# Kernel optimization log

Hardware: AMD Instinct MI355X
Metric: run time of the kernel (lower is better)

The kernel has to match this reference:

```python
import jax, jax.numpy as jnp
import numpy as np

HEADS = 4
DIM_HEAD = 32
SCALE = DIM_HEAD ** (-0.5)


def setup_inputs() -> dict:
    key = jax.random.key(0)
    k0, k1, k2 = jax.random.split(key, 3)
    B, C, H, W = 4, 256, 64, 64
    inner = HEADS * DIM_HEAD  # 128
    x = jax.random.normal(k0, (B, C, H, W), dtype=jnp.float32)
    # 1x1 conv weights reduce to matrices (out_ch, in_ch)
    w_qkv = jax.random.normal(k1, (3 * inner, C), dtype=jnp.float32) * 0.02
    w_out = jax.random.normal(k2, (C, inner), dtype=jnp.float32) * 0.02
    b_out = jnp.zeros((C,), dtype=jnp.float32)
    return {"x": x, "w_qkv": w_qkv, "w_out": w_out, "b_out": b_out}


def reference(x, w_qkv, w_out, b_out):
    b, c, h, w = x.shape
    n = h * w  # flattened spatial length
    inner = HEADS * DIM_HEAD
    # 1x1 conv == channel matmul: [b, 3*inner, h, w]
    qkv = jnp.einsum('oc,bchw->bohw', w_qkv, x)
    qkv = qkv.reshape(b, 3, HEADS, DIM_HEAD, n)  # split 3 * (heads dim_head)
    q, k, v = qkv[:, 0], qkv[:, 1], qkv[:, 2]    # each [b, heads, d, n]
    sim = jnp.einsum('bhdi,bhdj->bhij', q * SCALE, k)  # [b, h, n, n]
    attn = jax.nn.softmax(sim, axis=-1)  # stable (max-subtract) softmax
    out = jnp.einsum('bhij,bhdj->bhid', attn, v)       # [b, heads, n, d]
    # 'b h (x y) d -> b (h d) x y'
    out = out.transpose(0, 1, 3, 2).reshape(b, inner, h, w)
    y = jnp.einsum('oc,bchw->bohw', w_out, out) + b_out[None, :, None, None]
    return y
```

## Files before the change

### kernel.cpp

```cpp
#include <hip/hip_runtime.h>

#define N_TOK 4096
#define BATCH 4

typedef __attribute__((ext_vector_type(8))) short short8;
typedef __attribute__((ext_vector_type(4))) float floatx4;

__device__ __forceinline__ unsigned pack_rnd(float a, float b) {
    unsigned ra = __float_as_uint(a) + 0x8000u;
    unsigned rb = __float_as_uint(b) + 0x8000u;
    return __builtin_amdgcn_perm(rb, ra, 0x07060302u);
}

__device__ __forceinline__ void split_pack(float a, float b,
                                           unsigned &ph, unsigned &pl) {
    unsigned ra = __float_as_uint(a) + 0x8000u;
    unsigned rb = __float_as_uint(b) + 0x8000u;
    ph = __builtin_amdgcn_perm(rb, ra, 0x07060302u);
    float la = a - __uint_as_float(ra & 0xffff0000u);
    float lb = b - __uint_as_float(rb & 0xffff0000u);
    pl = __builtin_amdgcn_perm(__float_as_uint(lb) + 0x8000u,
                               __float_as_uint(la) + 0x8000u, 0x07060302u);
}

__device__ __forceinline__ short8 mk_short8(unsigned p0, unsigned p1,
                                            unsigned p2, unsigned p3) {
    union { unsigned u[4]; short8 s; } c;
    c.u[0] = p0; c.u[1] = p1; c.u[2] = p2; c.u[3] = p3;
    return c.s;
}

__device__ __forceinline__ void cvt_frag(const float* src,
                                         short8 &hi, short8 &lo) {
    float4 w0 = *(const float4*)src;
    float4 w1 = *(const float4*)(src + 4);
    unsigned ph[4], pl[4];
    split_pack(w0.x, w0.y, ph[0], pl[0]);
    split_pack(w0.z, w0.w, ph[1], pl[1]);
    split_pack(w1.x, w1.y, ph[2], pl[2]);
    split_pack(w1.z, w1.w, ph[3], pl[3]);
    hi = mk_short8(ph[0], ph[1], ph[2], ph[3]);
    lo = mk_short8(pl[0], pl[1], pl[2], pl[3]);
}

__device__ __forceinline__ float fast_exp2(float x) {
#if __has_builtin(__builtin_amdgcn_exp2f)
    return __builtin_amdgcn_exp2f(x);
#else
    return exp2f(x);
#endif
}

__global__ __launch_bounds__(256) void gemm1_fused(
    const float* __restrict__ wq, const float* __restrict__ x,
    unsigned short* __restrict__ Qp, unsigned short* __restrict__ Kp,
    unsigned short* __restrict__ Vp)
{
    const int N = N_TOK;
    const int b = blockIdx.z;
    const int row0 = blockIdx.y * 64;
    const int col0 = blockIdx.x * 64;
    const int t = threadIdx.x;
    const int wave = t >> 6, lane = t & 63;
    const int l16 = lane & 15, quad = lane >> 4;
    const int msub0 = (wave & 1) * 32, nsub0 = (wave >> 1) * 32;

    __shared__ __align__(16) char smem[29184];
    float (*Xf)[68] = (float(*)[68])smem;
    unsigned short* XsH = (unsigned short*)(smem + 8704);
    unsigned short* XsL = (unsigned short*)(smem + 13824);
    unsigned short* WsH = (unsigned short*)(smem + 18944);
    unsigned short* WsL = (unsigned short*)(smem + 24064);

    floatx4 acc[2][2] = {};

    const int xr = t >> 3, xnb = (t & 7) * 8;
    const int tnr = t >> 2, tkb = (t & 3) * 8;
    const int wm = t >> 2, wk = (t & 3) * 8;

    for (int kc = 0; kc < 8; ++kc) {
        __syncthreads();
        {
            const float* wsrc = wq + (size_t)(row0 + wm) * 256 + kc * 32 + wk;
            float4 w0 = *(const float4*)wsrc;
            float4 w1 = *(const float4*)(wsrc + 4);
            unsigned ph[4], pl[4];
            split_pack(w0.x, w0.y, ph[0], pl[0]);
            split_pack(w0.z, w0.w, ph[1], pl[1]);
            split_pack(w1.x, w1.y, ph[2], pl[2]);
            split_pack(w1.z, w1.w, ph[3], pl[3]);
            *(uint4*)(WsH + wm * 40 + wk) = *(uint4*)ph;
            *(uint4*)(WsL + wm * 40 + wk) = *(uint4*)pl;
        }
        {
            const float* src = x + ((size_t)b * 256 + kc * 32 + xr) * N + col0 + xnb;
            *(float4*)&Xf[xr][xnb]     = *(const float4*)src;
            *(float4*)&Xf[xr][xnb + 4] = *(const float4*)(src + 4);
        }
        __syncthreads();
        {
            unsigned ph[4], pl[4];
#pragma unroll
            for (int q = 0; q < 4; ++q)
                split_pack(Xf[tkb + 2 * q][tnr], Xf[tkb + 2 * q + 1][tnr],
                           ph[q], pl[q]);
            *(uint4*)(XsH + tnr * 40 + tkb) = *(uint4*)ph;
            *(uint4*)(XsL + tnr * 40 + tkb) = *(uint4*)pl;
        }
        __syncthreads();
        short8 ah0 = *(const short8*)(WsH + (msub0 + l16) * 40 + quad * 8);
        short8 ah1 = *(const short8*)(WsH + (msub0 + 16 + l16) * 40 + quad * 8);
        short8 al0 = *(const short8*)(WsL + (msub0 + l16) * 40 + quad * 8);
        short8 al1 = *(const short8*)(WsL + (msub0 + 16 + l16) * 40 + quad * 8);
        short8 bh0 = *(const short8*)(XsH + (nsub0 + l16) * 40 + quad * 8);
        short8 bh1 = *(const short8*)(XsH + (nsub0 + 16 + l16) * 40 + quad * 8);
        short8 bl0 = *(const short8*)(XsL + (nsub0 + l16) * 40 + quad * 8);
        short8 bl1 = *(const short8*)(XsL + (nsub0 + 16 + l16) * 40 + quad * 8);
        acc[0][0] = __builtin_amdgcn_mfma_f32_16x16x32_bf16(ah0, bh0, acc[0][0], 0, 0, 0);
        acc[0][1] = __builtin_amdgcn_mfma_f32_16x16x32_bf16(ah0, bh1, acc[0][1], 0, 0, 0);
        acc[1][0] = __builtin_amdgcn_mfma_f32_16x16x32_bf16(ah1, bh0, acc[1][0], 0, 0, 0);
        acc[1][1] = __builtin_amdgcn_mfma_f32_16x16x32_bf16(ah1, bh1, acc[1][1], 0, 0, 0);
        acc[0][0] = __builtin_amdgcn_mfma_f32_16x16x32_bf16(ah0, bl0, acc[0][0], 0, 0, 0);
        acc[0][1] = __builtin_amdgcn_mfma_f32_16x16x32_bf16(ah0, bl1, acc[0][1], 0, 0, 0);
        acc[1][0] = __builtin_amdgcn_mfma_f32_16x16x32_bf16(ah1, bl0, acc[1][0], 0, 0, 0);
        acc[1][1] = __builtin_amdgcn_mfma_f32_16x16x32_bf16(ah1, bl1, acc[1][1], 0, 0, 0);
        acc[0][0] = __builtin_amdgcn_mfma_f32_16x16x32_bf16(al0, bh0, acc[0][0], 0, 0, 0);
        acc[0][1] = __builtin_amdgcn_mfma_f32_16x16x32_bf16(al0, bh1, acc[0][1], 0, 0, 0);
        acc[1][0] = __builtin_amdgcn_mfma_f32_16x16x32_bf16(al1, bh0, acc[1][0], 0, 0, 0);
        acc[1][1] = __builtin_amdgcn_mfma_f32_16x16x32_bf16(al1, bh1, acc[1][1], 0, 0, 0);
    }

    __syncthreads();
    const int region = row0 >> 7;
    if (region == 2) {
        float (*LdsF)[68] = (float(*)[68])smem;
#pragma unroll
        for (int i = 0; i < 2; ++i)
#pragma unroll
            for (int j = 0; j < 2; ++j) {
                const int m = msub0 + i * 16 + quad * 4;
                const int n = nsub0 + j * 16 + l16;
#pragma unroll
                for (int r = 0; r < 4; ++r) LdsF[m + r][n] = acc[i][j][r];
            }
        __syncthreads();
        const int m = t >> 2, nb2 = (t & 3) * 16;
        const int vrow = b * 128 + (row0 - 256) + m;
        unsigned pk[8];
#pragma unroll
        for (int q = 0; q < 8; ++q)
            pk[q] = pack_rnd(LdsF[m][nb2 + 2 * q], LdsF[m][nb2 + 2 * q + 1]);
        unsigned short* dst = Vp + (size_t)vrow * N + col0 + nb2;
        *(uint4*)&dst[0] = *(uint4*)&pk[0];
        *(uint4*)&dst[8] = *(uint4*)&pk[4];
    } else {
        unsigned short (*LdsT)[68] = (unsigned short(*)[68])smem;
        const float sc = region ? 1.0f
                                : (0.17677669529663687f * 1.4426950408889634f);
#pragma unroll
        for (int i = 0; i < 2; ++i)
#pragma unroll
            for (int j = 0; j < 2; ++j) {
                const int m = msub0 + i * 16 + quad * 4;
                const int n = nsub0 + j * 16 + l16;
                uint2 pr;
                pr.x = pack_rnd(acc[i][j][0] * sc, acc[i][j][1] * sc);
                pr.y = pack_rnd(acc[i][j][2] * sc, acc[i][j][3] * sc);
                *(uint2*)&LdsT[n][m] = pr;
            }
        __syncthreads();
        const int n = t & 63, hb = (t >> 6) & 1, dh = t >> 7;
        const int h = ((row0 & 127) >> 5) + hb;
        const int m0 = hb * 32 + dh * 16;
        unsigned tmp[8];
        *(uint2*)&tmp[0] = *(const uint2*)&LdsT[n][m0];
        *(uint2*)&tmp[2] = *(const uint2*)&LdsT[n][m0 + 4];
        *(uint2*)&tmp[4] = *(const uint2*)&LdsT[n][m0 + 8];
        *(uint2*)&tmp[6] = *(const uint2*)&LdsT[n][m0 + 12];
        unsigned short* dst = (region ? Kp : Qp) +
            ((size_t)(b * 4 + h) * N + col0 + n) * 32 + dh * 16;
        *(uint4*)&dst[0] = *(uint4*)&tmp[0];
        *(uint4*)&dst[8] = *(uint4*)&tmp[4];
    }
}

__global__ __launch_bounds__(512) void attn_fused(
    const unsigned short* __restrict__ Qp,
    const unsigned short* __restrict__ Kp,
    const unsigned short* __restrict__ Vp,
    unsigned short* __restrict__ Oth, unsigned short* __restrict__ Otl)
{
    const int N = N_TOK;
    const int bh = blockIdx.y;
    const int b = bh >> 2, h = bh & 3;
    const int i0 = blockIdx.x * 128;
    const int t = threadIdx.x;
    const int wave = t >> 6, lane = t & 63;
    const int l16 = lane & 15, quad = lane >> 4;
    const int team = wave >> 2, w4 = wave & 3;

    __shared__ __align__(16) char smem[38912];
    unsigned short* S = (unsigned short*)smem;

    short8 ones;
#pragma unroll
    for (int e = 0; e < 8; ++e) ones[e] = (short)0x3F80;

    short8 qh[2];
#pragma unroll
    for (int g = 0; g < 2; ++g)
        qh[g] = *(const short8*)(Qp +
            ((size_t)bh * N + i0 + w4 * 32 + g * 16 + l16) * 32 + quad * 8);

    floatx4 o[2][2] = {};
    floatx4 lacc[2] = {};

    const int st_k = t & 255;
    const int skey = st_k >> 2, sdp = (st_k & 3) * 8;
    const int sslot = (skey & 32) | ((skey & 4) << 2) | ((skey & 24) >> 1)
                    | (skey & 3);
    const int svd = st_k >> 3, svp = (st_k & 7) * 8;
    const unsigned short* kp0 = Kp + ((size_t)bh * N + skey) * 32 + sdp;
    const unsigned short* kp1 = kp0 + (size_t)2048 * 32;
    const unsigned short* vp0 = Vp + ((size_t)bh * 32 + svd) * N + svp;
    const unsigned short* vp1 = vp0 + 2048;

    short8 r0, r1;
    if (t < 256) { r0 = *(const short8*)kp0; r1 = *(const short8*)kp1; }
    else         { r0 = *(const short8*)vp0; r1 = *(const short8*)vp1; }
    if (t < 256) {
        *(short8*)(S + sslot * 40 + sdp) = r0;
        *(short8*)(S + 2560 + sslot * 40 + sdp) = r1;
    } else {
        *(short8*)(S + 10240 + svd * 72 + svp) = r0;
        *(short8*)(S + 10240 + 2304 + svd * 72 + svp) = r1;
    }
    kp0 += 64 * 32; kp1 += 64 * 32; vp0 += 64; vp1 += 64;
    if (t < 256) { r0 = *(const short8*)kp0; r1 = *(const short8*)kp1; }
    else         { r0 = *(const short8*)vp0; r1 = *(const short8*)vp1; }
    __syncthreads();

    for (int it = 0; it < 32; ++it) {
        const int cur = it & 1;
        if (it + 1 < 32) {
            const int nb = 1 - cur;
            if (t < 256) {
                *(short8*)(S + nb * 5120 + sslot * 40 + sdp) = r0;
                *(short8*)(S + nb * 5120 + 2560 + sslot * 40 + sdp) = r1;
            } else {
                *(short8*)(S + 10240 + nb * 4608 + svd * 72 + svp) = r0;
                *(short8*)(S + 10240 + nb * 4608 + 2304 + svd * 72 + svp) = r1;
            }
        }
        if (it + 2 < 32) {
            kp0 += 64 * 32; kp1 += 64 * 32; vp0 += 64; vp1 += 64;
            if (t < 256) { r0 = *(const short8*)kp0; r1 = *(const short8*)kp1; }
            else         { r0 = *(const short8*)vp0; r1 = *(const short8*)vp1; }
        }

        const unsigned short* Ksr = S + cur * 5120 + team * 2560;
        const unsigned short* Vsr = S + 10240 + cur * 4608 + team * 2304;

        short8 kh0 = *(const short8*)(Ksr + ( 0 + l16) * 40 + quad * 8);
        short8 kh1 = *(const short8*)(Ksr + (16 + l16) * 40 + quad * 8);
        short8 kh2 = *(const short8*)(Ksr + (32 + l16) * 40 + quad * 8);
        short8 kh3 = *(const short8*)(Ksr + (48 + l16) * 40 + quad * 8);
        short8 vh00 = *(const short8*)(Vsr + ( 0 + l16) * 72 +  0 + quad * 8);
        short8 vh01 = *(const short8*)(Vsr + (16 + l16) * 72 +  0 + quad * 8);
        short8 vh10 = *(const short8*)(Vsr + ( 0 + l16) * 72 + 32 + quad * 8);
        short8 vh11 = *(const short8*)(Vsr + (16 + l16) * 72 + 32 + quad * 8);

#pragma unroll
        for (int g = 0; g < 2; ++g) {
            const floatx4 z = {0.0f, 0.0f, 0.0f, 0.0f};
            floatx4 s0 = __builtin_amdgcn_mfma_f32_16x16x32_bf16(kh0, qh[g], z, 0, 0, 0);
            floatx4 s1 = __builtin_amdgcn_mfma_f32_16x16x32_bf16(kh1, qh[g], z, 0, 0, 0);
            floatx4 s2 = __builtin_amdgcn_mfma_f32_16x16x32_bf16(kh2, qh[g], z, 0, 0, 0);
            floatx4 s3 = __builtin_amdgcn_mfma_f32_16x16x32_bf16(kh3, qh[g], z, 0, 0, 0);
            short8 pf0 = mk_short8(
                pack_rnd(fast_exp2(s0[0]), fast_exp2(s0[1])),
                pack_rnd(fast_exp2(s0[2]), fast_exp2(s0[3])),
                pack_rnd(fast_exp2(s1[0]), fast_exp2(s1[1])),
                pack_rnd(fast_exp2(s1[2]), fast_exp2(s1[3])));
            o[g][0] = __builtin_amdgcn_mfma_f32_16x16x32_bf16(vh00, pf0, o[g][0], 0, 0, 0);
            o[g][1] = __builtin_amdgcn_mfma_f32_16x16x32_bf16(vh01, pf0, o[g][1], 0, 0, 0);
            lacc[g] = __builtin_amdgcn_mfma_f32_16x16x32_bf16(ones, pf0, lacc[g], 0, 0, 0);
            short8 pf1 = mk_short8(
                pack_rnd(fast_exp2(s2[0]), fast_exp2(s2[1])),
                pack_rnd(fast_exp2(s2[2]), fast_exp2(s2[3])),
                pack_rnd(fast_exp2(s3[0]), fast_exp2(s3[1])),
                pack_rnd(fast_exp2(s3[2]), fast_exp2(s3[3])));
            o[g][0] = __builtin_amdgcn_mfma_f32_16x16x32_bf16(vh10, pf1, o[g][0], 0, 0, 0);
            o[g][1] = __builtin_amdgcn_mfma_f32_16x16x32_bf16(vh11, pf1, o[g][1], 0, 0, 0);
            lacc[g] = __builtin_amdgcn_mfma_f32_16x16x32_bf16(ones, pf1, lacc[g], 0, 0, 0);
        }
        __syncthreads();
    }

    float (*OfB)[132] = (float(*)[132])smem;
    float* Lb = (float*)(smem + 16896);
    float (*OfA)[132] = (float(*)[132])(smem + 17408);

    if (team == 1) {
#pragma unroll
        for (int g = 0; g < 2; ++g) {
            const int q = w4 * 32 + g * 16 + l16;
#pragma unroll
            for (int half = 0; half < 2; ++half)
#pragma unroll
                for (int r = 0; r < 4; ++r)
                    OfB[half * 16 + quad * 4 + r][q] = o[g][half][r];
            if (quad == 0) Lb[q] = lacc[g][0];
        }
    }
    __syncthreads();
    if (team == 0) {
#pragma unroll
        for (int g = 0; g < 2; ++g) {
            const int q = w4 * 32 + g * 16 + l16;
            const float inv = 1.0f / (lacc[g][0] + Lb[q]);
#pragma unroll
            for (int half = 0; half < 2; ++half)
#pragma unroll
                for (int r = 0; r < 4; ++r) {
                    const int d = half * 16 + quad * 4 + r;
                    OfA[d][q] = (o[g][half][r] + OfB[d][q]) * inv;
                }
        }
    }
    __syncthreads();
    {
        const int q = t >> 2, db = (t & 3) * 8;
        unsigned ph[4], pl[4];
#pragma unroll
        for (int i = 0; i < 4; ++i)
            split_pack(OfA[db + 2 * i][q], OfA[db + 2 * i + 1][q], ph[i], pl[i]);
        const size_t off = ((size_t)b * N + i0 + q) * 128 + h * 32 + db;
        *(uint4*)(Oth + off) = *(uint4*)ph;
        *(uint4*)(Otl + off) = *(uint4*)pl;
    }
}

__global__ __launch_bounds__(256) void gemm2_fused(
    const float* __restrict__ wo,
    const unsigned short* __restrict__ Oth, const unsigned short* __restrict__ Otl,
    const float* __restrict__ bias, float* __restrict__ y)
{
    const int N = N_TOK;
    const int b = blockIdx.z;
    const int row0 = blockIdx.y * 64;
    const int col0 = blockIdx.x * 64;
    const int t = threadIdx.x;
    const int wave = t >> 6, lane = t & 63;
    const int l16 = lane & 15, quad = lane >> 4;
    const int msub0 = (wave & 1) * 32, nsub0 = (wave >> 1) * 32;

    __shared__ __align__(16) char smem[17408];
    unsigned short* BsH = (unsigned short*)smem;
    unsigned short* BsL = (unsigned short*)(smem + 5120);
    float (*LdsF)[68] = (float(*)[68])smem;

    short8 ah[4][2], al[4][2];
#pragma unroll
    for (int kc = 0; kc < 4; ++kc)
#pragma unroll
        for (int r = 0; r < 2; ++r)
            cvt_frag(wo + (size_t)(row0 + msub0 + r * 16 + l16) * 128 +
                         kc * 32 + quad * 8,
                     ah[kc][r], al[kc][r]);

    const int srow = t >> 2, sk = (t & 3) * 8;
    const unsigned short* gH = Oth + ((size_t)b * N + col0 + srow) * 128 + sk;
    const unsigned short* gL = Otl + ((size_t)b * N + col0 + srow) * 128 + sk;

    floatx4 acc[2][2] = {};
#pragma unroll
    for (int kc = 0; kc < 4; ++kc) {
        short8 hreg = *(const short8*)(gH + kc * 32);
        short8 lreg = *(const short8*)(gL + kc * 32);
        __syncthreads();
        *(short8*)(BsH + srow * 40 + sk) = hreg;
        *(short8*)(BsL + srow * 40 + sk) = lreg;
        __syncthreads();
        short8 bh0 = *(const short8*)(BsH + (nsub0 + l16) * 40 + quad * 8);
        short8 bh1 = *(const short8*)(BsH + (nsub0 + 16 + l16) * 40 + quad * 8);
        short8 bl0 = *(const short8*)(BsL + (nsub0 + l16) * 40 + quad * 8);
        short8 bl1 = *(const short8*)(BsL + (nsub0 + 16 + l16) * 40 + quad * 8);
        acc[0][0] = __builtin_amdgcn_mfma_f32_16x16x32_bf16(ah[kc][0], bh0, acc[0][0], 0, 0, 0);
        acc[0][1] = __builtin_amdgcn_mfma_f32_16x16x32_bf16(ah[kc][0], bh1, acc[0][1], 0, 0, 0);
        acc[1][0] = __builtin_amdgcn_mfma_f32_16x16x32_bf16(ah[kc][1], bh0, acc[1][0], 0, 0, 0);
        acc[1][1] = __builtin_amdgcn_mfma_f32_16x16x32_bf16(ah[kc][1], bh1, acc[1][1], 0, 0, 0);
        acc[0][0] = __builtin_amdgcn_mfma_f32_16x16x32_bf16(ah[kc][0], bl0, acc[0][0], 0, 0, 0);
        acc[0][1] = __builtin_amdgcn_mfma_f32_16x16x32_bf16(ah[kc][0], bl1, acc[0][1], 0, 0, 0);
        acc[1][0] = __builtin_amdgcn_mfma_f32_16x16x32_bf16(ah[kc][1], bl0, acc[1][0], 0, 0, 0);
        acc[1][1] = __builtin_amdgcn_mfma_f32_16x16x32_bf16(ah[kc][1], bl1, acc[1][1], 0, 0, 0);
        acc[0][0] = __builtin_amdgcn_mfma_f32_16x16x32_bf16(al[kc][0], bh0, acc[0][0], 0, 0, 0);
        acc[0][1] = __builtin_amdgcn_mfma_f32_16x16x32_bf16(al[kc][0], bh1, acc[0][1], 0, 0, 0);
        acc[1][0] = __builtin_amdgcn_mfma_f32_16x16x32_bf16(al[kc][1], bh0, acc[1][0], 0, 0, 0);
        acc[1][1] = __builtin_amdgcn_mfma_f32_16x16x32_bf16(al[kc][1], bh1, acc[1][1], 0, 0, 0);
    }

    __syncthreads();
#pragma unroll
    for (int i = 0; i < 2; ++i)
#pragma unroll
        for (int j = 0; j < 2; ++j) {
            const int m = msub0 + i * 16 + quad * 4;
            const int n = nsub0 + j * 16 + l16;
#pragma unroll
            for (int r = 0; r < 4; ++r) LdsF[m + r][n] = acc[i][j][r];
        }
    __syncthreads();
    const int m = t >> 2, nb = (t & 3) * 16;
    const float bv = bias[row0 + m];
    float* dst = y + ((size_t)b * 256 + row0 + m) * N + col0 + nb;
#pragma unroll
    for (int g = 0; g < 4; ++g) {
        float4 o4;
        o4.x = LdsF[m][nb + g * 4 + 0] + bv;
        o4.y = LdsF[m][nb + g * 4 + 1] + bv;
        o4.z = LdsF[m][nb + g * 4 + 2] + bv;
        o4.w = LdsF[m][nb + g * 4 + 3] + bv;
        *(float4*)(dst + g * 4) = o4;
    }
}

extern "C" void kernel_launch(void* const* d_in, const int* in_sizes, int n_in,
                              void* d_out, int out_size, void* d_ws, size_t ws_size,
                              hipStream_t stream) {
    const float* x     = (const float*)d_in[0];
    const float* w_qkv = (const float*)d_in[1];
    const float* w_out = (const float*)d_in[2];
    const float* b_out = (const float*)d_in[3];
    float* y = (float*)d_out;

    char* base = (char*)d_ws;
    unsigned short* Qp  = (unsigned short*)base;
    unsigned short* Kp  = Qp + (size_t)16 * N_TOK * 32;
    unsigned short* Vp  = Kp + (size_t)16 * N_TOK * 32;
    unsigned short* Oth = Vp + (size_t)16 * N_TOK * 32;
    unsigned short* Otl = Oth + (size_t)BATCH * N_TOK * 128;

    gemm1_fused<<<dim3(64, 6, BATCH), dim3(256), 0, stream>>>(
        w_qkv, x, Qp, Kp, Vp);
    attn_fused<<<dim3(32, 16), dim3(512), 0, stream>>>(Qp, Kp, Vp, Oth, Otl);
    gemm2_fused<<<dim3(64, 4, BATCH), dim3(256), 0, stream>>>(
        w_out, Oth, Otl, b_out, y);
}
```

Baseline: 156.6 us.

## Pre-split weights and transpose x into bf16 hi/lo buffers before QKV GEMM

Adds prep kernels that convert w_qkv, w_out and x into bf16 hi/lo pairs ahead of time, with x transposed to token-major layout. A new gemm1_pre kernel then runs a double-buffered LDS pipeline over the pre-split operands instead of converting fp32 inside the GEMM. gemm2 loads the pre-split w_out directly. This removes repeated per-block conversion work, at the cost of two extra launches and an extra write and read of a transposed copy of x through workspace memory. The new path only runs when the workspace is large enough; otherwise the old kernels are used.

```diff
diff --git a/kernel.cpp b/kernel.cpp
--- a/kernel.cpp
+++ b/kernel.cpp
@@ -49,6 +49,200 @@
 #else
     return exp2f(x);
 #endif
+}
+
+__global__ __launch_bounds__(256) void prep_w(
+    const float* __restrict__ wq, const float* __restrict__ wo,
+    unsigned short* __restrict__ WqH, unsigned short* __restrict__ WqL,
+    unsigned short* __restrict__ WoH, unsigned short* __restrict__ WoL)
+{
+    const int u = blockIdx.x * 256 + threadIdx.x;
+    const float* src;
+    unsigned short *dh, *dl;
+    int e;
+    if (u < 12288) { src = wq; dh = WqH; dl = WqL; e = u * 8; }
+    else           { src = wo; dh = WoH; dl = WoL; e = (u - 12288) * 8; }
+    float4 w0 = *(const float4*)(src + e);
+    float4 w1 = *(const float4*)(src + e + 4);
+    unsigned ph[4], pl[4];
+    split_pack(w0.x, w0.y, ph[0], pl[0]);
+    split_pack(w0.z, w0.w, ph[1], pl[1]);
+    split_pack(w1.x, w1.y, ph[2], pl[2]);
+    split_pack(w1.z, w1.w, ph[3], pl[3]);
+    *(uint4*)(dh + e) = *(uint4*)ph;
+    *(uint4*)(dl + e) = *(uint4*)pl;
+}
+
+__global__ __launch_bounds__(256) void prep_x(
+    const float* __restrict__ x,
+    unsigned short* __restrict__ XtH, unsigned short* __restrict__ XtL)
+{
+    const int N = N_TOK;
+    const int n0 = blockIdx.x * 32;
+    const int b  = blockIdx.y;
+    const int t  = threadIdx.x;
+
+    __shared__ unsigned LdsH[32][132];
+    __shared__ unsigned LdsL[32][132];
+
+    const int pr = t >> 3;
+    const int ns = t & 7;
+#pragma unroll
+    for (int p = 0; p < 4; ++p) {
+        const int c = p * 64 + pr * 2;
+        const float* s0 = x + ((size_t)(b * 256 + c)) * N + n0 + ns * 4;
+        float4 a  = *(const float4*)s0;
+        float4 bb = *(const float4*)(s0 + N);
+        unsigned hd[4], ld[4];
+        split_pack(a.x, bb.x, hd[0], ld[0]);
+        split_pack(a.y, bb.y, hd[1], ld[1]);
+        split_pack(a.z, bb.z, hd[2], ld[2]);
+        split_pack(a.w, bb.w, hd[3], ld[3]);
+        const int cd = p * 32 + pr;
+#pragma unroll
+        for (int i = 0; i < 4; ++i) {
+            LdsH[ns * 4 + i][cd] = hd[i];
+            LdsL[ns * 4 + i][cd] = ld[i];
+        }
+    }
+    __syncthreads();
+    const int n = t >> 3, dq = (t & 7) * 16;
+    unsigned* XH = (unsigned*)XtH;
+    unsigned* XL = (unsigned*)XtL;
+    const size_t base = ((size_t)b * N + n0 + n) * 128 + dq;
+#pragma unroll
+    for (int j = 0; j < 4; ++j) {
+        *(uint4*)(XH + base + j * 4) = *(uint4*)&LdsH[n][dq + j * 4];
+        *(uint4*)(XL + base + j * 4) = *(uint4*)&LdsL[n][dq + j * 4];
+    }
+}
+
+__global__ __launch_bounds__(256) void gemm1_pre(
+    const unsigned short* __restrict__ WqH, const unsigned short* __restrict__ WqL,
+    const unsigned short* __restrict__ XtH, const unsigned short* __restrict__ XtL,
+    unsigned short* __restrict__ Qp, unsigned short* __restrict__ Kp,
+    unsigned short* __restrict__ Vp)
+{
+    const int N = N_TOK;
+    const int b = blockIdx.z;
+    const int row0 = blockIdx.y * 64;
+    const int col0 = blockIdx.x * 64;
+    const int t = threadIdx.x;
+    const int wave = t >> 6, lane = t & 63;
+    const int l16 = lane & 15, quad = lane >> 4;
+    const int msub0 = (wave & 1) * 32, nsub0 = (wave >> 1) * 32;
+
+    __shared__ __align__(16) char smem[40960];
+    unsigned short* S = (unsigned short*)smem;
+
+    const int m = t >> 2, kb = (t & 3) * 8;
+    const unsigned short* wqh = WqH + (size_t)(row0 + m) * 256 + kb;
+    const unsigned short* wql = WqL + (size_t)(row0 + m) * 256 + kb;
+    const unsigned short* xth = XtH + ((size_t)b * N + col0 + m) * 256 + kb;
+    const unsigned short* xtl = XtL + ((size_t)b * N + col0 + m) * 256 + kb;
+
+    floatx4 acc[2][2] = {};
+
+    {
+        short8 rwh = *(const short8*)wqh;
+        short8 rwl = *(const short8*)wql;
+        short8 rxh = *(const short8*)xth;
+        short8 rxl = *(const short8*)xtl;
+        *(short8*)(S +        m * 40 + kb) = rwh;
+        *(short8*)(S + 2560 + m * 40 + kb) = rwl;
+        *(short8*)(S + 5120 + m * 40 + kb) = rxh;
+        *(short8*)(S + 7680 + m * 40 + kb) = rxl;
+    }
+    __syncthreads();
+
+    for (int kc = 0; kc < 8; ++kc) {
+        const int cur = kc & 1;
+        if (kc + 1 < 8) {
+            short8 rwh = *(const short8*)(wqh + (kc + 1) * 32);
+            short8 rwl = *(const short8*)(wql + (kc + 1) * 32);
+            short8 rxh = *(const short8*)(xth + (kc + 1) * 32);
+            short8 rxl = *(const short8*)(xtl + (kc + 1) * 32);
+            unsigned short* D = S + (1 - cur) * 10240;
+            *(short8*)(D +        m * 40 + kb) = rwh;
+            *(short8*)(D + 2560 + m * 40 + kb) = rwl;
+            *(short8*)(D + 5120 + m * 40 + kb) = rxh;
+            *(short8*)(D + 7680 + m * 40 + kb) = rxl;
+        }
+        const unsigned short* B0 = S + cur * 10240;
+        short8 ah0 = *(const short8*)(B0 +        (msub0 +      l16) * 40 + quad * 8);
+        short8 ah1 = *(const short8*)(B0 +        (msub0 + 16 + l16) * 40 + quad * 8);
+        short8 al0 = *(const short8*)(B0 + 2560 + (msub0 +      l16) * 40 + quad * 8);
+        short8 al1 = *(const short8*)(B0 + 2560 + (msub0 + 16 + l16) * 40 + quad * 8);
+        short8 bh0 = *(const short8*)(B0 + 5120 + (nsub0 +      l16) * 40 + quad * 8);
+        short8 bh1 = *(const short8*)(B0 + 5120 + (nsub0 + 16 + l16) * 40 + quad * 8);
+        short8 bl0 = *(const short8*)(B0 + 7680 + (nsub0 +      l16) * 40 + quad * 8);
+        short8 bl1 = *(const short8*)(B0 + 7680 + (nsub0 + 16 + l16) * 40 + quad * 8);
+        acc[0][0] = __builtin_amdgcn_mfma_f32_16x16x32_bf16(ah0, bh0, acc[0][0], 0, 0, 0);
+        acc[0][1] = __builtin_amdgcn_mfma_f32_16x16x32_bf16(ah0, bh1, acc[0][1], 0, 0, 0);
+        acc[1][0] = __builtin_amdgcn_mfma_f32_16x16x32_bf16(ah1, bh0, acc[1][0], 0, 0, 0);
+        acc[1][1] = __builtin_amdgcn_mfma_f32_16x16x32_bf16(ah1, bh1, acc[1][1], 0, 0, 0);
+        acc[0][0] = __builtin_amdgcn_mfma_f32_16x16x32_bf16(ah0, bl0, acc[0][0], 0, 0, 0);
+        acc[0][1] = __builtin_amdgcn_mfma_f32_16x16x32_bf16(ah0, bl1, acc[0][1], 0, 0, 0);
+        acc[1][0] = __builtin_amdgcn_mfma_f32_16x16x32_bf16(ah1, bl0, acc[1][0], 0, 0, 0);
+        acc[1][1] = __builtin_amdgcn_mfma_f32_16x16x32_bf16(ah1, bl1, acc[1][1], 0, 0, 0);
+        acc[0][0] = __builtin_amdgcn_mfma_f32_16x16x32_bf16(al0, bh0, acc[0][0], 0, 0, 0);
+        acc[0][1] = __builtin_amdgcn_mfma_f32_16x16x32_bf16(al0, bh1, acc[0][1], 0, 0, 0);
+        acc[1][0] = __builtin_amdgcn_mfma_f32_16x16x32_bf16(al1, bh0, acc[1][0], 0, 0, 0);
+        acc[1][1] = __builtin_amdgcn_mfma_f32_16x16x32_bf16(al1, bh1, acc[1][1], 0, 0, 0);
+        __syncthreads();
+    }
+
+    const int region = row0 >> 7;
+    if (region == 2) {
+        float (*LdsF)[68] = (float(*)[68])smem;
+#pragma unroll
+        for (int i = 0; i < 2; ++i)
+#pragma unroll
+            for (int j = 0; j < 2; ++j) {
+                const int mm = msub0 + i * 16 + quad * 4;
+                const int n = nsub0 + j * 16 + l16;
+#pragma unroll
+                for (int r = 0; r < 4; ++r) LdsF[mm + r][n] = acc[i][j][r];
+            }
+        __syncthreads();
+        const int mm = t >> 2, nb2 = (t & 3) * 16;
+        const int vrow = b * 128 + (row0 - 256) + mm;
+        unsigned pk[8];
+#pragma unroll
+        for (int q = 0; q < 8; ++q)
+            pk[q] = pack_rnd(LdsF[mm][nb2 + 2 * q], LdsF[mm][nb2 + 2 * q + 1]);
+        unsigned short* dst = Vp + (size_t)vrow * N + col0 + nb2;
+        *(uint4*)&dst[0] = *(uint4*)&pk[0];
+        *(uint4*)&dst[8] = *(uint4*)&pk[4];
+    } else {
+        unsigned short (*LdsT)[68] = (unsigned short(*)[68])smem;
+        const float sc = region ? 1.0f
+                                : (0.17677669529663687f * 1.4426950408889634f);
+#pragma unroll
+        for (int i = 0; i < 2; ++i)
+#pragma unroll
+            for (int j = 0; j < 2; ++j) {
+                const int mm = msub0 + i * 16 + quad * 4;
+                const int n = nsub0 + j * 16 + l16;
+                uint2 pr;
+                pr.x = pack_rnd(acc[i][j][0] * sc, acc[i][j][1] * sc);
+                pr.y = pack_rnd(acc[i][j][2] * sc, acc[i][j][3] * sc);
+                *(uint2*)&LdsT[n][mm] = pr;
+            }
+        __syncthreads();
+        const int n = t & 63, hb = (t >> 6) & 1, dh = t >> 7;
+        const int h = ((row0 & 127) >> 5) + hb;
+        const int m0 = hb * 32 + dh * 16;
+        unsigned tmp[8];
+        *(uint2*)&tmp[0] = *(const uint2*)&LdsT[n][m0];
+        *(uint2*)&tmp[2] = *(const uint2*)&LdsT[n][m0 + 4];
+        *(uint2*)&tmp[4] = *(const uint2*)&LdsT[n][m0 + 8];
+        *(uint2*)&tmp[6] = *(const uint2*)&LdsT[n][m0 + 12];
+        unsigned short* dst = (region ? Kp : Qp) +
+            ((size_t)(b * 4 + h) * N + col0 + n) * 32 + dh * 16;
+        *(uint4*)&dst[0] = *(uint4*)&tmp[0];
+        *(uint4*)&dst[8] = *(uint4*)&tmp[4];
+    }
 }
 
 __global__ __launch_bounds__(256) void gemm1_fused(
@@ -343,6 +537,8 @@
 
 __global__ __launch_bounds__(256) void gemm2_fused(
     const float* __restrict__ wo,
+    const unsigned short* __restrict__ WoH, const unsigned short* __restrict__ WoL,
+    const int use_pre,
     const unsigned short* __restrict__ Oth, const unsigned short* __restrict__ Otl,
     const float* __restrict__ bias, float* __restrict__ y)
 {
@@ -361,13 +557,25 @@
     float (*LdsF)[68] = (float(*)[68])smem;
 
     short8 ah[4][2], al[4][2];
-#pragma unroll
-    for (int kc = 0; kc < 4; ++kc)
-#pragma unroll
-        for (int r = 0; r < 2; ++r)
-            cvt_frag(wo + (size_t)(row0 + msub0 + r * 16 + l16) * 128 +
-                         kc * 32 + quad * 8,
-                     ah[kc][r], al[kc][r]);
+    if (use_pre) {
+#pragma unroll
+        for (int kc = 0; kc < 4; ++kc)
+#pragma unroll
+            for (int r = 0; r < 2; ++r) {
+                const size_t off = (size_t)(row0 + msub0 + r * 16 + l16) * 128 +
+                                   kc * 32 + quad * 8;
+                ah[kc][r] = *(const short8*)(WoH + off);
+                al[kc][r] = *(const short8*)(WoL + off);
+            }
+    } else {
+#pragma unroll
+        for (int kc = 0; kc < 4; ++kc)
+#pragma unroll
+            for (int r = 0; r < 2; ++r)
+                cvt_frag(wo + (size_t)(row0 + msub0 + r * 16 + l16) * 128 +
+                             kc * 32 + quad * 8,
+                         ah[kc][r], al[kc][r]);
+    }
 
     const int srow = t >> 2, sk = (t & 3) * 8;
     const unsigned short* gH = Oth + ((size_t)b * N + col0 + srow) * 128 + sk;
@@ -435,15 +643,38 @@
     float* y = (float*)d_out;
 
     char* base = (char*)d_ws;
-    unsigned short* Qp  = (unsigned short*)base;
-    unsigned short* Kp  = Qp + (size_t)16 * N_TOK * 32;
-    unsigned short* Vp  = Kp + (size_t)16 * N_TOK * 32;
-    unsigned short* Oth = Vp + (size_t)16 * N_TOK * 32;
-    unsigned short* Otl = Oth + (size_t)BATCH * N_TOK * 128;
-
-    gemm1_fused<<<dim3(64, 6, BATCH), dim3(256), 0, stream>>>(
-        w_qkv, x, Qp, Kp, Vp);
-    attn_fused<<<dim3(32, 16), dim3(512), 0, stream>>>(Qp, Kp, Vp, Oth, Otl);
-    gemm2_fused<<<dim3(64, 4, BATCH), dim3(256), 0, stream>>>(
-        w_out, Oth, Otl, b_out, y);
-}
+    unsigned short* Qp = (unsigned short*)base;
+    unsigned short* Kp = Qp + (size_t)16 * N_TOK * 32;
+    unsigned short* Vp = Kp + (size_t)16 * N_TOK * 32;
+
+    const size_t NEED = 29884416;
+    if (ws_size >= NEED) {
+        unsigned short* WqH = (unsigned short*)(base + 12582912);
+        unsigned short* WqL = WqH + 98304;
+        unsigned short* WoH = WqL + 98304;
+        unsigned short* WoL = WoH + 32768;
+        unsigned short* XtH = (unsigned short*)(base + 13107200);
+        unsigned short* XtL = (unsigned short*)(base + 21495808);
+        unsigned short* Oth = (unsigned short*)(base + 13107200);
+        unsigned short* Otl = Oth + (size_t)BATCH * N_TOK * 128;
+
+        prep_w<<<dim3(64), dim3(256), 0, stream>>>(
+            w_qkv, w_out, WqH, WqL, WoH, WoL);
+        prep_x<<<dim3(128, BATCH), dim3(256), 0, stream>>>(x, XtH, XtL);
+        gemm1_pre<<<dim3(64, 6, BATCH), dim3(256), 0, stream>>>(
+            WqH, WqL, XtH, XtL, Qp, Kp, Vp);
+        attn_fused<<<dim3(32, 16), dim3(512), 0, stream>>>(
+            Qp, Kp, Vp, Oth, Otl);
+        gemm2_fused<<<dim3(64, 4, BATCH), dim3(256), 0, stream>>>(
+            w_out, WoH, WoL, 1, Oth, Otl, b_out, y);
+    } else {
+        unsigned short* Oth = (unsigned short*)(base + 12582912);
+        unsigned short* Otl = Oth + (size_t)BATCH * N_TOK * 128;
+        gemm1_fused<<<dim3(64, 6, BATCH), dim3(256), 0, stream>>>(
+            w_qkv, x, Qp, Kp, Vp);
+        attn_fused<<<dim3(32, 16), dim3(512), 0, stream>>>(
+            Qp, Kp, Vp, Oth, Otl);
+        gemm2_fused<<<dim3(64, 4, BATCH), dim3(256), 0, stream>>>(
+            w_out, nullptr, nullptr, 0, Oth, Otl, b_out, y);
+    }
+}
```

Measured after the change: 163.1 us. 4.2% more time.
